# Optimization experiments

Hardware: AMD Instinct MI355X
Metric: run time of the kernel (lower is better)

Reference implementation:

```python
import jax, jax.numpy as jnp
import numpy as np

N, E = 50000, 800000
IN, OUT, H, B = 512, 512, 8, 4  # num_bases=4, aggregators=['symnorm'] (PyG EGConv defaults)
FH = OUT // H  # per-head dim = 64
EPS = 1e-5


def setup_inputs() -> dict:
    key = jax.random.key(0)
    ks = jax.random.split(key, 8)
    s_in = 1.0 / np.sqrt(IN)
    return {
        "x": jax.random.normal(ks[0], (N, IN), jnp.float32),
        "edge_index": jax.random.randint(ks[1], (2, E), 0, N, jnp.int32),
        "W_bases": jax.random.normal(ks[2], (IN, B * FH), jnp.float32) * s_in,  # bases_lin (no bias)
        "W_comb": jax.random.normal(ks[3], (IN, H * B), jnp.float32) * s_in,    # comb_lin weight
        "b_comb": jnp.zeros((H * B,), jnp.float32),                               # comb_lin bias
        "conv_bias": jnp.zeros((OUT,), jnp.float32),                              # EGConv output bias
        "W_res": jax.random.normal(ks[4], (IN, OUT), jnp.float32) * s_in,        # res_connection
        "b_res": jnp.zeros((OUT,), jnp.float32),
        "gamma": jnp.ones((OUT,), jnp.float32),                                   # LayerNorm weight
        "beta": jnp.zeros((OUT,), jnp.float32),                                   # LayerNorm bias
    }


def reference(x, edge_index, W_bases, W_comb, b_comb, conv_bias, W_res, b_res, gamma, beta):
    n = x.shape[0]
    # --- gcn_norm with self-loops (symnorm aggregator) ---
    loops = jnp.arange(n, dtype=edge_index.dtype)
    src = jnp.concatenate([edge_index[0], loops])  # [E+N]
    dst = jnp.concatenate([edge_index[1], loops])
    deg = jax.ops.segment_sum(jnp.ones_like(src, dtype=x.dtype), dst, num_segments=n)
    dinv = jnp.where(deg > 0, jax.lax.rsqrt(jnp.maximum(deg, 1.0)), 0.0)
    norm = dinv[src] * dinv[dst]  # [E+N]

    # --- EGConv: bases projection, symnorm aggregation, per-head combination ---
    bases = x @ W_bases  # [N, B*FH]
    agg = jax.ops.segment_sum(bases[src] * norm[:, None], dst, num_segments=n)  # [N, B*FH]
    weightings = (x @ W_comb + b_comb).reshape(n, H, B)        # [N, H, B]  (num_aggrs=1)
    agg = agg.reshape(n, B, FH)                                  # [N, B, FH]
    conv_out = jnp.einsum('nhb,nbf->nhf', weightings, agg).reshape(n, OUT) + conv_bias

    # --- residual + LayerNorm + ReLU (dropout p=0 -> identity) ---
    out = conv_out + x @ W_res + b_res
    mu = out.mean(-1, keepdims=True)
    var = out.var(-1, keepdims=True)
    out = (out - mu) * jax.lax.rsqrt(var + EPS) * gamma + beta
    return jax.nn.relu(out)
```

## Files before the change

### kernel.cpp

```cpp
#include <hip/hip_runtime.h>
#include <hip/hip_bf16.h>

#define KDIM 512
#define ODIM 512
#define NB 4
#define NH 8
#define FH 64
#define BFH 256
#define HB 32
#define NCAT 896
#define COL_W 256
#define COL_R 288
#define LN_EPS 1e-5f
#define SCAN_BLK 1024

typedef __attribute__((ext_vector_type(8))) short short8;
typedef __attribute__((ext_vector_type(4))) float floatx4;

__device__ __forceinline__ float b2f(unsigned short u) {
    union { unsigned int i; float f; } v; v.i = ((unsigned int)u) << 16; return v.f;
}
__device__ __forceinline__ unsigned short f2b(float f) {
    __hip_bfloat16 h = __float2bfloat16(f);
    return *(unsigned short*)&h;
}
__device__ __forceinline__ void async16(const void* g, void* l) {
    __builtin_amdgcn_global_load_lds(
        (__attribute__((address_space(1))) unsigned int*)(g),
        (__attribute__((address_space(3))) unsigned int*)(l),
        16, 0, 0);
}

__global__ __launch_bounds__(256) void scan_sums_kernel(
        const int* __restrict__ deg, int* __restrict__ sums, int N) {
    int t = threadIdx.x;
    int idx = blockIdx.x * SCAN_BLK + t * 4;
    int4 v = {0, 0, 0, 0};
    if (idx + 3 < N) v = *(const int4*)(deg + idx);
    else {
        if (idx < N)     v.x = deg[idx];
        if (idx + 1 < N) v.y = deg[idx + 1];
        if (idx + 2 < N) v.z = deg[idx + 2];
        if (idx + 3 < N) v.w = deg[idx + 3];
    }
    int s = v.x + v.y + v.z + v.w;
    #pragma unroll
    for (int o = 32; o > 0; o >>= 1) s += __shfl_down(s, o, 64);
    __shared__ int ws[4];
    int lane = t & 63, w = t >> 6;
    if (lane == 0) ws[w] = s;
    __syncthreads();
    if (t == 0) sums[blockIdx.x] = ws[0] + ws[1] + ws[2] + ws[3];
}

__global__ __launch_bounds__(1024) void scan_base_kernel(
        int* __restrict__ sums, int nb) {
    __shared__ int sm[1024];
    int t = threadIdx.x;
    int own = (t < nb) ? sums[t] : 0;
    sm[t] = own;
    __syncthreads();
    for (int o = 1; o < 1024; o <<= 1) {
        int u = (t >= o) ? sm[t - o] : 0;
        __syncthreads();
        sm[t] += u;
        __syncthreads();
    }
    if (t < nb) sums[t] = sm[t] - own;
}

__global__ __launch_bounds__(256) void scan_write_kernel(
        const int* __restrict__ deg, const int* __restrict__ bases,
        int* __restrict__ offsets, int* __restrict__ woff,
        float* __restrict__ dinv, int N, int E) {
    int t = threadIdx.x;
    int idx = blockIdx.x * SCAN_BLK + t * 4;
    int4 v = {0, 0, 0, 0};
    if (idx + 3 < N) v = *(const int4*)(deg + idx);
    else {
        if (idx < N)     v.x = deg[idx];
        if (idx + 1 < N) v.y = deg[idx + 1];
        if (idx + 2 < N) v.z = deg[idx + 2];
        if (idx + 3 < N) v.w = deg[idx + 3];
    }
    int s = v.x + v.y + v.z + v.w;
    __shared__ int sm[256];
    sm[t] = s;
    __syncthreads();
    for (int o = 1; o < 256; o <<= 1) {
        int u = (t >= o) ? sm[t - o] : 0;
        __syncthreads();
        sm[t] += u;
        __syncthreads();
    }
    int o0 = sm[t] - s + bases[blockIdx.x];
    int o1 = o0 + v.x, o2 = o1 + v.y, o3 = o2 + v.z;
    if (idx + 3 < N) {
        int4 ov = {o0, o1, o2, o3};
        *(int4*)(offsets + idx) = ov;
        *(int4*)(woff + idx) = ov;
        float4 dv = {rsqrtf((float)v.x + 1.0f), rsqrtf((float)v.y + 1.0f),
                     rsqrtf((float)v.z + 1.0f), rsqrtf((float)v.w + 1.0f)};
        *(float4*)(dinv + idx) = dv;
    } else {
        int oo[4] = {o0, o1, o2, o3};
        int vv[4] = {v.x, v.y, v.z, v.w};
        for (int j = 0; j < 4; j++) {
            if (idx + j < N) {
                offsets[idx + j] = oo[j];
                woff[idx + j] = oo[j];
                dinv[idx + j] = rsqrtf((float)vv[j] + 1.0f);
            }
        }
    }
    if (blockIdx.x == 0 && t == 0) offsets[N] = E;
}

__global__ void fill_kernel(const int* __restrict__ src, const int* __restrict__ dst,
                            int* __restrict__ woff, int* __restrict__ ebuf, int E) {
    int i = blockIdx.x * blockDim.x + threadIdx.x;
    if (i < E) {
        int pos = atomicAdd(&woff[dst[i]], 1);
        ebuf[pos] = src[i];
    }
}

__global__ __launch_bounds__(256) void prep_kernel(
        const float* __restrict__ x, unsigned short* __restrict__ xb, long total4,
        int nCvtBlocks, int nStageBlocks,
        const float* __restrict__ Wb, const float* __restrict__ Wc,
        const float* __restrict__ Wr, const float* __restrict__ bcomb,
        const float* __restrict__ bres,
        unsigned short* __restrict__ wT, float* __restrict__ bias_cat,
        const int* __restrict__ dst, int* __restrict__ deg, int E) {
    int blk = blockIdx.x;
    if (blk < nCvtBlocks) {
        long i = (long)blk * 256 + threadIdx.x;
        if (i >= total4) return;
        float4 v = ((const float4*)x)[i];
        ushort4 u;
        u.x = f2b(v.x); u.y = f2b(v.y); u.z = f2b(v.z); u.w = f2b(v.w);
        ((ushort4*)xb)[i] = u;
    } else if (blk < nCvtBlocks + nStageBlocks) {
        int idx = (blk - nCvtBlocks) * 256 + threadIdx.x;
        if (idx >= NCAT * KDIM) return;
        int c = idx >> 9, k = idx & (KDIM - 1);
        float v;
        if (c < BFH)                   v = Wb[(size_t)k * BFH + c];
        else if (c < COL_R)            v = Wc[(size_t)k * HB + (c - COL_W)];
        else if (c < COL_R + ODIM)     v = Wr[(size_t)k * ODIM + (c - COL_R)];
        else                           v = 0.0f;
        wT[(size_t)c * KDIM + k] = f2b(v);
        if (k == 0) {
            float bv = 0.0f;
            if (c >= COL_W && c < COL_R)             bv = bcomb[c - COL_W];
            else if (c >= COL_R && c < COL_R + ODIM) bv = bres[c - COL_R];
            bias_cat[c] = bv;
        }
    } else {
        int i = (blk - nCvtBlocks - nStageBlocks) * 256 + threadIdx.x;
        if (i < E) atomicAdd(&deg[dst[i]], 1);
    }
}

#define BM 128
#define BN 128
#define BK 32
#define SLD 136

__global__ __launch_bounds__(256) void mfma_gemm_kernel(
        const unsigned short* __restrict__ xb,
        const unsigned short* __restrict__ wT,
        const float* __restrict__ bias_cat,
        unsigned short* __restrict__ Cb,
        int N) {
    __shared__ short lds[8192];
    short* As0 = lds;
    short* As1 = lds + 4096;
    int t = threadIdx.x;
    int l = t & 63, w = t >> 6;
    int wr = w >> 1, wc = w & 1;
    int quad = l >> 4, m = l & 15;

    int nwg = gridDim.x;
    int orig = blockIdx.x;
    int q = nwg >> 3, r = nwg & 7;
    int xcd = orig & 7, slot = orig >> 3;
    int wg = (xcd < r) ? (xcd * (q + 1) + slot)
                       : (r * (q + 1) + (xcd - r) * q + slot);
    int bx = wg % 7, by = wg / 7;
    int row0 = by * BM;
    int col0 = bx * BN;

    floatx4 acc[4][4];
    floatx4 zero4 = {0.f, 0.f, 0.f, 0.f};
    #pragma unroll
    for (int i = 0; i < 4; i++)
        #pragma unroll
        for (int j = 0; j < 4; j++) acc[i][j] = zero4;

    int ar0 = row0 + (w << 4) + (l >> 2);
    int ar1 = ar0 + 64;
    int kk = (l & 3) * 8;
    const unsigned short* agp0 = xb + (size_t)min(ar0, N - 1) * KDIM + kk;
    const unsigned short* agp1 = xb + (size_t)min(ar1, N - 1) * KDIM + kk;
    const unsigned short* bq[4];
    #pragma unroll
    for (int j = 0; j < 4; j++)
        bq[j] = wT + (size_t)(col0 + wc * 64 + j * 16 + m) * KDIM + quad * 8;

    auto stage = [&](short* A, int k0) {
        async16(agp0 + k0, A + w * 512);
        async16(agp1 + k0, A + 2048 + w * 512);
    };
    auto compute = [&](const short* As, int k0) {
        short8 a[4], b[4];
        #pragma unroll
        for (int j = 0; j < 4; j++)
            b[j] = *(const short8*)(bq[j] + k0);
        #pragma unroll
        for (int i = 0; i < 4; i++)
            a[i] = *(const short8*)(As + (wr * 64 + i * 16 + m) * BK + quad * 8);
        #pragma unroll
        for (int i = 0; i < 4; i++)
            #pragma unroll
            for (int j = 0; j < 4; j++)
                acc[i][j] = __builtin_amdgcn_mfma_f32_16x16x32_bf16(
                    a[i], b[j], acc[i][j], 0, 0, 0);
    };

    stage(As0, 0);
    __syncthreads();

    for (int k0 = 0; k0 < KDIM; k0 += 2 * BK) {
        if (k0 + BK < KDIM) stage(As1, k0 + BK);
        compute(As0, k0);
        __syncthreads();
        if (k0 + 2 * BK < KDIM) stage(As0, k0 + 2 * BK);
        compute(As1, k0 + BK);
        __syncthreads();
    }

    float bj[4];
    #pragma unroll
    for (int j = 0; j < 4; j++) bj[j] = bias_cat[col0 + wc * 64 + j * 16 + m];

    unsigned short* stage_buf = (unsigned short*)lds;
    #pragma unroll
    for (int i = 0; i < 4; i++) {
        __syncthreads();
        #pragma unroll
        for (int j = 0; j < 4; j++)
            #pragma unroll
            for (int r2 = 0; r2 < 4; r2++)
                stage_buf[(wr * 16 + quad * 4 + r2) * SLD + wc * 64 + j * 16 + m] =
                    f2b(acc[i][j][r2] + bj[j]);
        __syncthreads();
        #pragma unroll
        for (int u = t; u < 512; u += 256) {
            int lr = u >> 4, c8 = u & 15;
            int gr = row0 + ((lr & 16) ? 64 : 0) + i * 16 + (lr & 15);
            if (gr < N) {
                int4 v = *(const int4*)(stage_buf + lr * SLD + c8 * 8);
                *(int4*)(Cb + (size_t)gr * NCAT + col0 + c8 * 8) = v;
            }
        }
    }
}

__global__ __launch_bounds__(256) void gather_combine_kernel(
        const int* __restrict__ offsets, const int* __restrict__ ebuf,
        const float* __restrict__ dinv, const unsigned short* __restrict__ Cb,
        const float* __restrict__ conv_bias, const float* __restrict__ gamma,
        const float* __restrict__ beta, float* __restrict__ out, int N) {
    __shared__ float sagg[4][BFH];
    int wave = (blockIdx.x * blockDim.x + threadIdx.x) >> 6;
    int lane = threadIdx.x & 63;
    int wib = (threadIdx.x >> 6);
    if (wave >= N) return;
    int n = wave;
    float di = dinv[n];
    float self = di * di;
    ushort4 u = ((const ushort4*)(Cb + (size_t)n * NCAT))[lane];
    float ax = b2f(u.x) * self, ay = b2f(u.y) * self;
    float az = b2f(u.z) * self, aw = b2f(u.w) * self;
    int e = offsets[n], end = offsets[n + 1];
    for (; e + 8 <= end; e += 8) {
        int s0 = ebuf[e + 0], s1 = ebuf[e + 1], s2 = ebuf[e + 2], s3 = ebuf[e + 3];
        int s4 = ebuf[e + 4], s5 = ebuf[e + 5], s6 = ebuf[e + 6], s7 = ebuf[e + 7];
        float w0 = dinv[s0] * di, w1 = dinv[s1] * di;
        float w2 = dinv[s2] * di, w3 = dinv[s3] * di;
        float w4 = dinv[s4] * di, w5 = dinv[s5] * di;
        float w6 = dinv[s6] * di, w7 = dinv[s7] * di;
        ushort4 u0 = ((const ushort4*)(Cb + (size_t)s0 * NCAT))[lane];
        ushort4 u1 = ((const ushort4*)(Cb + (size_t)s1 * NCAT))[lane];
        ushort4 u2 = ((const ushort4*)(Cb + (size_t)s2 * NCAT))[lane];
        ushort4 u3 = ((const ushort4*)(Cb + (size_t)s3 * NCAT))[lane];
        ushort4 u4 = ((const ushort4*)(Cb + (size_t)s4 * NCAT))[lane];
        ushort4 u5 = ((const ushort4*)(Cb + (size_t)s5 * NCAT))[lane];
        ushort4 u6 = ((const ushort4*)(Cb + (size_t)s6 * NCAT))[lane];
        ushort4 u7 = ((const ushort4*)(Cb + (size_t)s7 * NCAT))[lane];
        ax += b2f(u0.x) * w0 + b2f(u1.x) * w1 + b2f(u2.x) * w2 + b2f(u3.x) * w3
            + b2f(u4.x) * w4 + b2f(u5.x) * w5 + b2f(u6.x) * w6 + b2f(u7.x) * w7;
        ay += b2f(u0.y) * w0 + b2f(u1.y) * w1 + b2f(u2.y) * w2 + b2f(u3.y) * w3
            + b2f(u4.y) * w4 + b2f(u5.y) * w5 + b2f(u6.y) * w6 + b2f(u7.y) * w7;
        az += b2f(u0.z) * w0 + b2f(u1.z) * w1 + b2f(u2.z) * w2 + b2f(u3.z) * w3
            + b2f(u4.z) * w4 + b2f(u5.z) * w5 + b2f(u6.z) * w6 + b2f(u7.z) * w7;
        aw += b2f(u0.w) * w0 + b2f(u1.w) * w1 + b2f(u2.w) * w2 + b2f(u3.w) * w3
            + b2f(u4.w) * w4 + b2f(u5.w) * w5 + b2f(u6.w) * w6 + b2f(u7.w) * w7;
    }
    if (e < end) {
        int last = end - 1;
        int s0 = ebuf[min(e + 0, last)], s1 = ebuf[min(e + 1, last)];
        int s2 = ebuf[min(e + 2, last)], s3 = ebuf[min(e + 3, last)];
        int s4 = ebuf[min(e + 4, last)], s5 = ebuf[min(e + 5, last)];
        int s6 = ebuf[min(e + 6, last)], s7 = ebuf[min(e + 7, last)];
        float w0 = (e + 0 < end) ? dinv[s0] * di : 0.0f;
        float w1 = (e + 1 < end) ? dinv[s1] * di : 0.0f;
        float w2 = (e + 2 < end) ? dinv[s2] * di : 0.0f;
        float w3 = (e + 3 < end) ? dinv[s3] * di : 0.0f;
        float w4 = (e + 4 < end) ? dinv[s4] * di : 0.0f;
        float w5 = (e + 5 < end) ? dinv[s5] * di : 0.0f;
        float w6 = (e + 6 < end) ? dinv[s6] * di : 0.0f;
        float w7 = (e + 7 < end) ? dinv[s7] * di : 0.0f;
        ushort4 u0 = ((const ushort4*)(Cb + (size_t)s0 * NCAT))[lane];
        ushort4 u1 = ((const ushort4*)(Cb + (size_t)s1 * NCAT))[lane];
        ushort4 u2 = ((const ushort4*)(Cb + (size_t)s2 * NCAT))[lane];
        ushort4 u3 = ((const ushort4*)(Cb + (size_t)s3 * NCAT))[lane];
        ushort4 u4 = ((const ushort4*)(Cb + (size_t)s4 * NCAT))[lane];
        ushort4 u5 = ((const ushort4*)(Cb + (size_t)s5 * NCAT))[lane];
        ushort4 u6 = ((const ushort4*)(Cb + (size_t)s6 * NCAT))[lane];
        ushort4 u7 = ((const ushort4*)(Cb + (size_t)s7 * NCAT))[lane];
        ax += b2f(u0.x) * w0 + b2f(u1.x) * w1 + b2f(u2.x) * w2 + b2f(u3.x) * w3
            + b2f(u4.x) * w4 + b2f(u5.x) * w5 + b2f(u6.x) * w6 + b2f(u7.x) * w7;
        ay += b2f(u0.y) * w0 + b2f(u1.y) * w1 + b2f(u2.y) * w2 + b2f(u3.y) * w3
            + b2f(u4.y) * w4 + b2f(u5.y) * w5 + b2f(u6.y) * w6 + b2f(u7.y) * w7;
        az += b2f(u0.z) * w0 + b2f(u1.z) * w1 + b2f(u2.z) * w2 + b2f(u3.z) * w3
            + b2f(u4.z) * w4 + b2f(u5.z) * w5 + b2f(u6.z) * w6 + b2f(u7.z) * w7;
        aw += b2f(u0.w) * w0 + b2f(u1.w) * w1 + b2f(u2.w) * w2 + b2f(u3.w) * w3
            + b2f(u4.w) * w4 + b2f(u5.w) * w5 + b2f(u6.w) * w6 + b2f(u7.w) * w7;
    }
    float4 av = {ax, ay, az, aw};
    *(float4*)(&sagg[wib][lane * 4]) = av;

    int h = lane >> 3;
    int f0 = (lane & 7) * 8;
    int t0 = lane * 8;
    const unsigned short* crow = Cb + (size_t)n * NCAT;
    ushort4 wu = *(const ushort4*)(crow + COL_W + h * 4);
    float cw0 = b2f(wu.x), cw1 = b2f(wu.y), cw2 = b2f(wu.z), cw3 = b2f(wu.w);

    float4 b0a = *(const float4*)(&sagg[wib][0 * FH + f0]);
    float4 b0b = *(const float4*)(&sagg[wib][0 * FH + f0 + 4]);
    float4 b1a = *(const float4*)(&sagg[wib][1 * FH + f0]);
    float4 b1b = *(const float4*)(&sagg[wib][1 * FH + f0 + 4]);
    float4 b2a = *(const float4*)(&sagg[wib][2 * FH + f0]);
    float4 b2b = *(const float4*)(&sagg[wib][2 * FH + f0 + 4]);
    float4 b3a = *(const float4*)(&sagg[wib][3 * FH + f0]);
    float4 b3b = *(const float4*)(&sagg[wib][3 * FH + f0 + 4]);
    float a0[8] = {b0a.x, b0a.y, b0a.z, b0a.w, b0b.x, b0b.y, b0b.z, b0b.w};
    float a1[8] = {b1a.x, b1a.y, b1a.z, b1a.w, b1b.x, b1b.y, b1b.z, b1b.w};
    float a2[8] = {b2a.x, b2a.y, b2a.z, b2a.w, b2b.x, b2b.y, b2b.z, b2b.w};
    float a3[8] = {b3a.x, b3a.y, b3a.z, b3a.w, b3b.x, b3b.y, b3b.z, b3b.w};

    short8 rv = *(const short8*)(crow + COL_R + t0);
    float4 cb0 = *(const float4*)(conv_bias + t0);
    float4 cb1 = *(const float4*)(conv_bias + t0 + 4);
    float cb[8] = {cb0.x, cb0.y, cb0.z, cb0.w, cb1.x, cb1.y, cb1.z, cb1.w};

    float v[8];
    float s = 0.f, s2 = 0.f;
    #pragma unroll
    for (int j = 0; j < 8; j++) {
        float conv = cw0 * a0[j] + cw1 * a1[j] + cw2 * a2[j] + cw3 * a3[j];
        float val = conv + cb[j] + b2f((unsigned short)rv[j]);
        v[j] = val;
        s += val;
        s2 += val * val;
    }
    #pragma unroll
    for (int o = 32; o > 0; o >>= 1) {
        s  += __shfl_xor(s, o, 64);
        s2 += __shfl_xor(s2, o, 64);
    }
    float mu = s * (1.0f / (float)ODIM);
    float var = s2 * (1.0f / (float)ODIM) - mu * mu;
    float rstd = rsqrtf(var + LN_EPS);

    float4 g0 = *(const float4*)(gamma + t0);
    float4 g1 = *(const float4*)(gamma + t0 + 4);
    float4 be0 = *(const float4*)(beta + t0);
    float4 be1 = *(const float4*)(beta + t0 + 4);
    float g[8] = {g0.x, g0.y, g0.z, g0.w, g1.x, g1.y, g1.z, g1.w};
    float be[8] = {be0.x, be0.y, be0.z, be0.w, be1.x, be1.y, be1.z, be1.w};

    float ov[8];
    #pragma unroll
    for (int j = 0; j < 8; j++) {
        float o = (v[j] - mu) * rstd * g[j] + be[j];
        ov[j] = fmaxf(o, 0.0f);
    }
    float4* op = (float4*)(out + (size_t)n * ODIM + t0);
    op[0] = make_float4(ov[0], ov[1], ov[2], ov[3]);
    op[1] = make_float4(ov[4], ov[5], ov[6], ov[7]);
}

static inline char* ws_alloc(char*& p, size_t bytes) {
    char* r = p;
    p += (bytes + 255) & ~(size_t)255;
    return r;
}

extern "C" void kernel_launch(void* const* d_in, const int* in_sizes, int n_in,
                              void* d_out, int out_size, void* d_ws, size_t ws_size,
                              hipStream_t stream) {
    const float* x         = (const float*)d_in[0];
    const int*   ei        = (const int*)d_in[1];
    const float* W_bases   = (const float*)d_in[2];
    const float* W_comb    = (const float*)d_in[3];
    const float* b_comb    = (const float*)d_in[4];
    const float* conv_bias = (const float*)d_in[5];
    const float* W_res     = (const float*)d_in[6];
    const float* b_res     = (const float*)d_in[7];
    const float* gamma     = (const float*)d_in[8];
    const float* beta      = (const float*)d_in[9];

    int N = in_sizes[0] / KDIM;
    int E = in_sizes[1] / 2;
    const int* src = ei;
    const int* dst = ei + E;
    int nScanBlocks = (N + SCAN_BLK - 1) / SCAN_BLK;

    char* p = (char*)d_ws;
    int*   deg      = (int*)ws_alloc(p, sizeof(int) * (size_t)N);
    int*   offsets  = (int*)ws_alloc(p, sizeof(int) * (size_t)(N + 1));
    int*   woff     = (int*)ws_alloc(p, sizeof(int) * (size_t)N);
    int*   ebuf     = (int*)ws_alloc(p, sizeof(int) * (size_t)E);
    int*   sums     = (int*)ws_alloc(p, sizeof(int) * (size_t)nScanBlocks);
    float* dinv     = (float*)ws_alloc(p, sizeof(float) * (size_t)N);
    float* bias_cat = (float*)ws_alloc(p, sizeof(float) * NCAT);
    unsigned short* Cb  = (unsigned short*)ws_alloc(p, 2ull * N * NCAT);
    unsigned short* xb  = (unsigned short*)ws_alloc(p, 2ull * N * KDIM);
    unsigned short* wT  = (unsigned short*)ws_alloc(p, 2ull * NCAT * KDIM);
    float* out = (float*)d_out;

    hipMemsetAsync(deg, 0, sizeof(int) * (size_t)N, stream);

    long total4 = (long)N * KDIM / 4;
    int nCvtBlocks = (int)((total4 + 255) / 256);
    int nStageBlocks = (NCAT * KDIM + 255) / 256;
    int nDegBlocks = (E + 255) / 256;
    prep_kernel<<<nCvtBlocks + nStageBlocks + nDegBlocks, 256, 0, stream>>>(
        x, xb, total4, nCvtBlocks, nStageBlocks, W_bases, W_comb, W_res,
        b_comb, b_res, wT, bias_cat, dst, deg, E);

    scan_sums_kernel<<<nScanBlocks, 256, 0, stream>>>(deg, sums, N);
    scan_base_kernel<<<1, 1024, 0, stream>>>(sums, nScanBlocks);
    scan_write_kernel<<<nScanBlocks, 256, 0, stream>>>(deg, sums, offsets, woff,
                                                       dinv, N, E);
    fill_kernel<<<(E + 255) / 256, 256, 0, stream>>>(src, dst, woff, ebuf, E);

    int nYB = (N + BM - 1) / BM;
    mfma_gemm_kernel<<<7 * nYB, 256, 0, stream>>>(xb, wT, bias_cat, Cb, N);

    gather_combine_kernel<<<(N + 3) / 4, 256, 0, stream>>>(
        offsets, ebuf, dinv, Cb, conv_bias, gamma, beta, out, N);
}
```

Baseline: 457.4 us.

## Stage B tiles through LDS with XOR-swizzled layout in MFMA GEMM

The weight (B) operand of the bf16 MFMA GEMM was previously read straight from global memory by every wave on each k-step. It is now loaded asynchronously into double-buffered LDS alongside A. Both A and B tiles use an XOR swizzle on the 8-element k-chunks so the 16-byte LDS reads avoid bank conflicts. This doubles LDS use per block, which may reduce occupancy.

```diff
diff --git a/kernel.cpp b/kernel.cpp
--- a/kernel.cpp
+++ b/kernel.cpp
@@ -174,9 +174,11 @@
         const float* __restrict__ bias_cat,
         unsigned short* __restrict__ Cb,
         int N) {
-    __shared__ short lds[8192];
+    __shared__ short lds[16384];
     short* As0 = lds;
-    short* As1 = lds + 4096;
+    short* Bs0 = lds + 4096;
+    short* As1 = lds + 8192;
+    short* Bs1 = lds + 12288;
     int t = threadIdx.x;
     int l = t & 63, w = t >> 6;
     int wr = w >> 1, wc = w & 1;
@@ -201,26 +203,28 @@
 
     int ar0 = row0 + (w << 4) + (l >> 2);
     int ar1 = ar0 + 64;
-    int kk = (l & 3) * 8;
+    int brow = col0 + (w << 4) + (l >> 2);
+    int kk = (((l & 3) ^ ((l >> 2) & 3)) * 8);
     const unsigned short* agp0 = xb + (size_t)min(ar0, N - 1) * KDIM + kk;
     const unsigned short* agp1 = xb + (size_t)min(ar1, N - 1) * KDIM + kk;
-    const unsigned short* bq[4];
-    #pragma unroll
-    for (int j = 0; j < 4; j++)
-        bq[j] = wT + (size_t)(col0 + wc * 64 + j * 16 + m) * KDIM + quad * 8;
-
-    auto stage = [&](short* A, int k0) {
+    const unsigned short* bgp0 = wT + (size_t)brow * KDIM + kk;
+    const unsigned short* bgp1 = bgp0 + (size_t)64 * KDIM;
+
+    auto stage = [&](short* A, short* B, int k0) {
         async16(agp0 + k0, A + w * 512);
         async16(agp1 + k0, A + 2048 + w * 512);
+        async16(bgp0 + k0, B + w * 512);
+        async16(bgp1 + k0, B + 2048 + w * 512);
     };
-    auto compute = [&](const short* As, int k0) {
+    auto compute = [&](const short* As, const short* Bs) {
+        int qs = (quad ^ (m & 3)) * 8;
         short8 a[4], b[4];
         #pragma unroll
+        for (int i = 0; i < 4; i++)
+            a[i] = *(const short8*)(As + (wr * 64 + i * 16 + m) * BK + qs);
+        #pragma unroll
         for (int j = 0; j < 4; j++)
-            b[j] = *(const short8*)(bq[j] + k0);
-        #pragma unroll
-        for (int i = 0; i < 4; i++)
-            a[i] = *(const short8*)(As + (wr * 64 + i * 16 + m) * BK + quad * 8);
+            b[j] = *(const short8*)(Bs + (wc * 64 + j * 16 + m) * BK + qs);
         #pragma unroll
         for (int i = 0; i < 4; i++)
             #pragma unroll
@@ -229,15 +233,15 @@
                     a[i], b[j], acc[i][j], 0, 0, 0);
     };
 
-    stage(As0, 0);
+    stage(As0, Bs0, 0);
     __syncthreads();
 
     for (int k0 = 0; k0 < KDIM; k0 += 2 * BK) {
-        if (k0 + BK < KDIM) stage(As1, k0 + BK);
-        compute(As0, k0);
-        __syncthreads();
-        if (k0 + 2 * BK < KDIM) stage(As0, k0 + 2 * BK);
-        compute(As1, k0 + BK);
+        if (k0 + BK < KDIM) stage(As1, Bs1, k0 + BK);
+        compute(As0, Bs0);
+        __syncthreads();
+        if (k0 + 2 * BK < KDIM) stage(As0, Bs0, k0 + 2 * BK);
+        compute(As1, Bs1);
         __syncthreads();
     }
 
```

New measurement: 419.6 us. 8.3% less time.
